# Performance work log

Hardware: AMD Instinct MI355X
Metric: run time of the kernel (lower is better)

## Reference

```python
import jax, jax.numpy as jnp
import numpy as np

B, NB, K, C, CM, POS = 8, 1024, 9, 32, 128, 2
SIGMA = 0.5
NEG_SLOPE = 0.01  # nn.LeakyReLU default
BN_EPS = 1e-5


def _leaky(x):
    return jnp.where(x >= 0, x, NEG_SLOPE * x)


def _batchnorm(x, gamma, beta):
    # BatchNorm1d, training-mode batch statistics over the point dimension
    mu = jnp.mean(x, axis=0)
    var = jnp.mean((x - mu) ** 2, axis=0)
    return gamma * (x - mu) * jax.lax.rsqrt(var + BN_EPS) + beta


def setup_inputs() -> dict:
    key = jax.random.key(0)
    ks = jax.random.split(key, 8)
    N = B * NB
    positions = jax.random.normal(ks[0], (N, POS), jnp.float32)
    weights = jax.random.normal(ks[1], (N, C), jnp.float32)
    batch = jnp.full((B,), NB, dtype=jnp.int32)  # uniform point counts per graph
    # KernelConv params: kernel_init='grid' -> 3x3 grid of offsets spanning +-sigma
    g = jnp.linspace(-SIGMA, SIGMA, 3, dtype=jnp.float32)
    kernel_positions = jnp.stack(jnp.meshgrid(g, g, indexing='ij'), axis=-1).reshape(K, POS)
    kernel_weights = (jax.random.normal(ks[2], (K, C, C), jnp.float32) / np.float32(np.sqrt(C * K)))
    conv_norm_gamma = jnp.ones((C,), jnp.float32)
    conv_norm_beta = jnp.zeros((C,), jnp.float32)
    # PyG MLP([C, CM, C+POS], act_first=True, plain_last=True)
    W1 = jax.random.normal(ks[3], (C, CM), jnp.float32) / np.float32(np.sqrt(C))
    b1 = jnp.zeros((CM,), jnp.float32)
    bn_gamma = jnp.ones((CM,), jnp.float32)
    bn_beta = jnp.zeros((CM,), jnp.float32)
    W2 = jax.random.normal(ks[4], (CM, C + POS), jnp.float32) / np.float32(np.sqrt(CM))
    b2 = jnp.zeros((C + POS,), jnp.float32)
    return dict(positions=positions, weights=weights, batch=batch,
                kernel_positions=kernel_positions, kernel_weights=kernel_weights,
                conv_norm_gamma=conv_norm_gamma, conv_norm_beta=conv_norm_beta,
                W1=W1, b1=b1, bn_gamma=bn_gamma, bn_beta=bn_beta, W2=W2, b2=b2)


def reference(positions, weights, batch, kernel_positions, kernel_weights,
              conv_norm_gamma, conv_norm_beta, W1, b1, bn_gamma, bn_beta, W2, b2):
    N = positions.shape[0]
    # --- KernelConv: each point spawns K components at pos + kernel offset ---
    conv_pos = (positions[:, None, :] + kernel_positions[None, :, :])  # [N,K,2]
    conv_w = jnp.einsum('nc,kcd->nkd', weights, kernel_weights)        # [N,K,C]
    conv_pos = conv_pos.reshape(B, NB * K, POS)
    conv_w = conv_w.reshape(B, NB * K, C)
    # --- KernelSample: evaluate Gaussian mixture at original positions ---
    p = positions.reshape(B, NB, POS)
    d2 = (jnp.sum(p * p, -1)[:, :, None]
          + jnp.sum(conv_pos * conv_pos, -1)[:, None, :]
          - 2.0 * jnp.einsum('bnd,bmd->bnm', p, conv_pos))             # [B,NB,NB*K]
    Kmat = jnp.exp(-d2 / (2.0 * SIGMA * SIGMA))
    sampled = jnp.einsum('bnm,bmc->bnc', Kmat, conv_w).reshape(N, C)
    x = _leaky(sampled)                                                 # KernelSample nonlinearity
    # conv_norm + residual add of input weights
    x = _batchnorm(x, conv_norm_gamma, conv_norm_beta) + weights
    # MLP: lin -> act -> batchnorm (act_first) -> plain last lin
    h = _batchnorm(_leaky(x @ W1 + b1), bn_gamma, bn_beta)
    mlp_out = h @ W2 + b2                                               # [N, POS + C]
    delta_pos, delta_w = mlp_out[:, :POS], mlp_out[:, POS:]
    return positions + delta_pos, x + delta_w
```

## Files before the change

kernel.cpp:

```cpp
#include <hip/hip_runtime.h>
#include <hip/hip_bf16.h>

#define BB    8
#define NBB   1024
#define KK    9
#define CC    32
#define CMM   128
#define NTOT  (BB*NBB)
#define MM    (NBB*KK)
#define MS    16
#define MR    (MM/MS)
#define NEG   0.01f
#define EPS   1e-5f
#define L2C   (-2.8853900817779268f)

#define OFF_CWT   0
#define SZ_CWT    (BB*CC*MM/2)
#define OFF_CFX   (OFF_CWT + SZ_CWT)
#define OFF_CFY   (OFF_CFX + BB*MM)
#define OFF_CF0   (OFF_CFY + BB*MM)
#define OFF_PART  (OFF_CF0 + BB*MM)
#define SZ_ONE    (NTOT*CC)
#define SZ_PART   (MS*SZ_ONE)
#define OFF_X0    (OFF_PART)
#define OFF_X     (OFF_PART + SZ_ONE)
#define OFF_H0    (OFF_PART + 2*SZ_ONE)
#define OFF_ST    (OFF_PART + SZ_PART)

typedef __attribute__((ext_vector_type(8))) short short8;
typedef __attribute__((ext_vector_type(4))) float f32x4;
typedef __attribute__((ext_vector_type(2))) float f32x2;

static __device__ __forceinline__ unsigned short f2bf_rne(float f) {
    __hip_bfloat16 h = __float2bfloat16(f);
    return *reinterpret_cast<unsigned short*>(&h);
}

__global__ __launch_bounds__(256) void k_convw(const float* __restrict__ pos,
                                               const float* __restrict__ kpos,
                                               const float* __restrict__ w,
                                               const float* __restrict__ kw,
                                               float* __restrict__ cfx,
                                               float* __restrict__ cfy,
                                               float* __restrict__ cf0,
                                               float* __restrict__ stats,
                                               short* __restrict__ cwT) {
    __shared__ unsigned short tile[4*32*144];
    __shared__ unsigned short kwl[KK*CC*CC];
    int t = threadIdx.x;
    int l = t & 63, wv = t >> 6;
    int lane15 = l & 15, quad = l >> 4;
    int blk = blockIdx.x;
    int b = blk >> 4, nbl = blk & 15;
    int n = b*NBB + nbl*64 + wv*16 + lane15;

    if (blk == 0 && t < 320) stats[t] = 0.f;
    #pragma unroll
    for (int rep = 0; rep < 3; ++rep) {
        int gid = blk*256 + t + rep*32768;
        if (gid < BB*MM) {
            int bb = gid / MM;
            int m = gid - bb*MM;
            int np = m / 9, k9 = m - np*9;
            float qx = pos[((size_t)(bb*NBB + np))*2 + 0] + kpos[k9*2 + 0];
            float qy = pos[((size_t)(bb*NBB + np))*2 + 1] + kpos[k9*2 + 1];
            cfx[gid] = -2.f*L2C*qx;
            cfy[gid] = -2.f*L2C*qy;
            cf0[gid] = L2C*(qx*qx + qy*qy);
        }
    }

    for (int u = t; u < KK*CC*CC/4; u += 256) {
        int flat = u*4;
        int row  = flat >> 5;
        int c0   = flat & 31;
        int kk = row >> 5, cp = row & 31;
        f32x4 v = *(const f32x4*)&kw[flat];
        kwl[(kk*CC + c0+0)*CC + cp] = f2bf_rne(v.x);
        kwl[(kk*CC + c0+1)*CC + cp] = f2bf_rne(v.y);
        kwl[(kk*CC + c0+2)*CC + cp] = f2bf_rne(v.z);
        kwl[(kk*CC + c0+3)*CC + cp] = f2bf_rne(v.w);
    }

    f32x4 w0 = *(const f32x4*)&w[(size_t)n*CC + quad*8];
    f32x4 w1 = *(const f32x4*)&w[(size_t)n*CC + quad*8 + 4];
    union { unsigned short us[8]; short8 s; } bfr;
    bfr.us[0] = f2bf_rne(w0.x); bfr.us[1] = f2bf_rne(w0.y);
    bfr.us[2] = f2bf_rne(w0.z); bfr.us[3] = f2bf_rne(w0.w);
    bfr.us[4] = f2bf_rne(w1.x); bfr.us[5] = f2bf_rne(w1.y);
    bfr.us[6] = f2bf_rne(w1.z); bfr.us[7] = f2bf_rne(w1.w);

    __syncthreads();

    f32x4 acc[KK][2];
    #pragma unroll
    for (int kk = 0; kk < KK; ++kk) {
        #pragma unroll
        for (int ct = 0; ct < 2; ++ct) {
            int c = ct*16 + lane15;
            short8 afr = *(const short8*)&kwl[(kk*CC + c)*CC + quad*8];
            acc[kk][ct] = __builtin_amdgcn_mfma_f32_16x16x32_bf16(
                afr, bfr.s, (f32x4)0.f, 0, 0, 0);
        }
    }
    unsigned short* tw = tile + wv*4608;
    #pragma unroll
    for (int kk = 0; kk < KK; ++kk)
        #pragma unroll
        for (int ct = 0; ct < 2; ++ct)
            #pragma unroll
            for (int reg = 0; reg < 4; ++reg) {
                int c = ct*16 + quad*4 + reg;
                tw[c*144 + lane15*9 + kk] = f2bf_rne(acc[kk][ct][reg]);
            }
    __syncthreads();
    short* dst = cwT + (size_t)b*CC*MM + (size_t)(nbl*64 + wv*16)*9;
    #pragma unroll
    for (int it = 0; it < 9; ++it) {
        int u = it*64 + l;
        int c = u / 18, seg = u - c*18;
        short8 v = *(const short8*)&tw[c*144 + seg*8];
        *(short8*)&dst[(size_t)c*MM + seg*8] = v;
    }
}

__global__ __launch_bounds__(256) void k_sample(const float* __restrict__ pos,
                                                const float* __restrict__ cfx,
                                                const float* __restrict__ cfy,
                                                const float* __restrict__ cf0,
                                                const short* __restrict__ cwT,
                                                float* __restrict__ part) {
    int t = threadIdx.x;
    int l = t & 63, w = t >> 6;
    int blk = blockIdx.x;
    int ks = blk & 15, nb = (blk >> 4) & 7, b = blk >> 7;
    int lane15 = l & 15, quad = l >> 4;
    int nbase = b*NBB + nb*128 + w*32;

    float px[2], py[2], cn[2];
    #pragma unroll
    for (int nt = 0; nt < 2; ++nt) {
        int n = nbase + nt*16 + lane15;
        float x = pos[(size_t)n*2], y = pos[(size_t)n*2 + 1];
        px[nt] = x; py[nt] = y; cn[nt] = L2C*(x*x + y*y);
    }
    f32x4 acc[2][2];
    #pragma unroll
    for (int nt = 0; nt < 2; ++nt) { acc[nt][0] = (f32x4)0.f; acc[nt][1] = (f32x4)0.f; }

    const float* bx = cfx + (size_t)b*MM;
    const float* by = cfy + (size_t)b*MM;
    const float* b0 = cf0 + (size_t)b*MM;
    const short* ca0 = cwT + (size_t)b*CC*MM + (size_t)lane15*MM;
    const short* ca1 = ca0 + (size_t)16*MM;

    int m0 = ks*MR + quad*8;
    #pragma unroll 2
    for (int kk = 0; kk < MR/32; ++kk, m0 += 32) {
        short8 a0 = *(const short8*)&ca0[m0];
        short8 a1 = *(const short8*)&ca1[m0];
        f32x4 vx0 = *(const f32x4*)&bx[m0];
        f32x4 vx1 = *(const f32x4*)&bx[m0 + 4];
        f32x4 vy0 = *(const f32x4*)&by[m0];
        f32x4 vy1 = *(const f32x4*)&by[m0 + 4];
        f32x4 v00 = *(const f32x4*)&b0[m0];
        f32x4 v01 = *(const f32x4*)&b0[m0 + 4];
        #pragma unroll
        for (int nt = 0; nt < 2; ++nt) {
            f32x2 Xv = {px[nt], px[nt]};
            f32x2 Yv = {py[nt], py[nt]};
            f32x2 Cv = {cn[nt], cn[nt]};
            f32x2 t0 = (f32x2){v00.x, v00.y} + Cv;
            t0 = (f32x2){vy0.x, vy0.y}*Yv + t0;
            t0 = (f32x2){vx0.x, vx0.y}*Xv + t0;
            f32x2 t1 = (f32x2){v00.z, v00.w} + Cv;
            t1 = (f32x2){vy0.z, vy0.w}*Yv + t1;
            t1 = (f32x2){vx0.z, vx0.w}*Xv + t1;
            f32x2 t2 = (f32x2){v01.x, v01.y} + Cv;
            t2 = (f32x2){vy1.x, vy1.y}*Yv + t2;
            t2 = (f32x2){vx1.x, vx1.y}*Xv + t2;
            f32x2 t3 = (f32x2){v01.z, v01.w} + Cv;
            t3 = (f32x2){vy1.z, vy1.w}*Yv + t3;
            t3 = (f32x2){vx1.z, vx1.w}*Xv + t3;
            float e0 = __builtin_amdgcn_exp2f(t0.x);
            float e1 = __builtin_amdgcn_exp2f(t0.y);
            float e2 = __builtin_amdgcn_exp2f(t1.x);
            float e3 = __builtin_amdgcn_exp2f(t1.y);
            float e4 = __builtin_amdgcn_exp2f(t2.x);
            float e5 = __builtin_amdgcn_exp2f(t2.y);
            float e6 = __builtin_amdgcn_exp2f(t3.x);
            float e7 = __builtin_amdgcn_exp2f(t3.y);
            union { unsigned int u[4]; short8 s; } bf;
            bf.u[0] = (__float_as_uint(e0) >> 16) | (__float_as_uint(e1) & 0xffff0000u);
            bf.u[1] = (__float_as_uint(e2) >> 16) | (__float_as_uint(e3) & 0xffff0000u);
            bf.u[2] = (__float_as_uint(e4) >> 16) | (__float_as_uint(e5) & 0xffff0000u);
            bf.u[3] = (__float_as_uint(e6) >> 16) | (__float_as_uint(e7) & 0xffff0000u);
            acc[nt][0] = __builtin_amdgcn_mfma_f32_16x16x32_bf16(a0, bf.s, acc[nt][0], 0, 0, 0);
            acc[nt][1] = __builtin_amdgcn_mfma_f32_16x16x32_bf16(a1, bf.s, acc[nt][1], 0, 0, 0);
        }
    }
    #pragma unroll
    for (int nt = 0; nt < 2; ++nt) {
        int n = nbase + nt*16 + lane15;
        #pragma unroll
        for (int ct = 0; ct < 2; ++ct) {
            int c = ct*16 + quad*4;
            *(f32x4*)&part[((size_t)ks*NTOT + n)*CC + c] = acc[nt][ct];
        }
    }
}

__global__ __launch_bounds__(256) void k_leaky_stats(const float* __restrict__ part,
                                                     float* __restrict__ x0,
                                                     float* __restrict__ s1) {
    __shared__ float ss[32], sq[32];
    int t = threadIdx.x;
    if (t < 32) { ss[t] = 0.f; sq[t] = 0.f; }
    __syncthreads();
    float lsum = 0.f, lsq = 0.f;
    int base = blockIdx.x * 1024;
    for (int j = 0; j < 4; ++j) {
        int idx = base + j*256 + t;
        float v = 0.f;
        #pragma unroll
        for (int s = 0; s < MS; ++s) v += part[(size_t)s*SZ_ONE + idx];
        v = v >= 0.f ? v : NEG*v;
        x0[idx] = v;
        lsum += v; lsq = fmaf(v, v, lsq);
    }
    atomicAdd(&ss[t & 31], lsum);
    atomicAdd(&sq[t & 31], lsq);
    __syncthreads();
    if (t < 32) { atomicAdd(&s1[t], ss[t]); atomicAdd(&s1[32+t], sq[t]); }
}

__global__ __launch_bounds__(256) void k_mlp1(const float* __restrict__ x0,
                                              const float* __restrict__ wts,
                                              const float* __restrict__ gma,
                                              const float* __restrict__ bta,
                                              const float* __restrict__ W1,
                                              const float* __restrict__ b1,
                                              const float* __restrict__ s1,
                                              float* __restrict__ x,
                                              float* __restrict__ h0,
                                              float* __restrict__ s2) {
    __shared__ float tile[64*68];
    int t = threadIdx.x;
    int l = t & 63, w = t >> 6;
    int blk = blockIdx.x;
    int nb = blk >> 1, jh = blk & 1;
    int n = nb*64 + l;
    int j0 = jh*64 + w*16;

    float xv[32];
    #pragma unroll
    for (int c = 0; c < 32; ++c) {
        float mu  = s1[c] * (1.f/NTOT);
        float var = s1[32+c]*(1.f/NTOT) - mu*mu;
        float a   = gma[c] * rsqrtf(var + EPS);
        float v   = x0[(size_t)n*CC + c];
        xv[c] = a*(v - mu) + bta[c] + wts[(size_t)n*CC + c];
    }
    if (jh == 0 && w == 0) {
        #pragma unroll
        for (int c = 0; c < 32; c += 4)
            *(float4*)&x[(size_t)n*CC + c] = make_float4(xv[c], xv[c+1], xv[c+2], xv[c+3]);
    }
    float acc[16];
    #pragma unroll
    for (int jj = 0; jj < 16; ++jj) acc[jj] = b1[j0 + jj];
    #pragma unroll 4
    for (int c = 0; c < 32; ++c) {
        float xc = xv[c];
        const float* w1r = W1 + c*CMM + j0;
        #pragma unroll
        for (int jj = 0; jj < 16; ++jj)
            acc[jj] = fmaf(xc, w1r[jj], acc[jj]);
    }
    float* hd = h0 + (size_t)n*CMM + j0;
    #pragma unroll
    for (int jj = 0; jj < 16; ++jj) {
        acc[jj] = acc[jj] >= 0.f ? acc[jj] : NEG*acc[jj];
        tile[(w*16 + jj)*68 + l] = acc[jj];
    }
    #pragma unroll
    for (int jj = 0; jj < 16; jj += 4)
        *(float4*)&hd[jj] = make_float4(acc[jj], acc[jj+1], acc[jj+2], acc[jj+3]);
    __syncthreads();
    int jl = t >> 2, grp = t & 3;
    float lsum = 0.f, lsq = 0.f;
    #pragma unroll
    for (int q = 0; q < 4; ++q) {
        f32x4 v = *(const f32x4*)&tile[jl*68 + grp*16 + q*4];
        lsum += v.x + v.y + v.z + v.w;
        lsq = fmaf(v.x, v.x, fmaf(v.y, v.y, fmaf(v.z, v.z, fmaf(v.w, v.w, lsq))));
    }
    lsum += __shfl_xor(lsum, 1); lsq += __shfl_xor(lsq, 1);
    lsum += __shfl_xor(lsum, 2); lsq += __shfl_xor(lsq, 2);
    if (grp == 0) {
        int jg = jh*64 + jl;
        atomicAdd(&s2[jg], lsum);
        atomicAdd(&s2[CMM + jg], lsq);
    }
}

__global__ __launch_bounds__(256) void k_mlp2(const float* __restrict__ h0,
                                              const float* __restrict__ x,
                                              const float* __restrict__ pos,
                                              const float* __restrict__ g2,
                                              const float* __restrict__ bt2,
                                              const float* __restrict__ W2,
                                              const float* __restrict__ b2,
                                              const float* __restrict__ s2,
                                              float* __restrict__ out) {
    __shared__ float red[8][32][35];
    int t = threadIdx.x;
    int lane = t & 63, w = t >> 6;
    int half = lane >> 5;
    int nl = lane & 31;
    int n = blockIdx.x*32 + nl;
    int j0 = w*32 + half*16;
    float hv[16];
    #pragma unroll
    for (int q = 0; q < 4; ++q)
        *(float4*)&hv[q*4] = *(const float4*)&h0[(size_t)n*CMM + j0 + q*4];
    #pragma unroll
    for (int jj = 0; jj < 16; ++jj) {
        int j = j0 + jj;
        float mu  = s2[j] * (1.f/NTOT);
        float var = s2[CMM+j]*(1.f/NTOT) - mu*mu;
        float a   = g2[j] * rsqrtf(var + EPS);
        hv[jj] = a*(hv[jj] - mu) + bt2[j];
    }
    float acc[34];
    #pragma unroll
    for (int c = 0; c < 34; ++c) acc[c] = 0.f;
    for (int jj = 0; jj < 16; ++jj) {
        float h = hv[jj];
        const float* w2r = W2 + (size_t)(j0 + jj)*34;
        #pragma unroll
        for (int c = 0; c < 34; ++c)
            acc[c] = fmaf(h, w2r[c], acc[c]);
    }
    int rid = w*2 + half;
    #pragma unroll
    for (int c = 0; c < 34; ++c) red[rid][nl][c] = acc[c];
    __syncthreads();
    for (int u = t; u < 32*34; u += 256) {
        int r = u / 34, c = u - r*34;
        float v = red[0][r][c] + red[1][r][c] + red[2][r][c] + red[3][r][c]
                + red[4][r][c] + red[5][r][c] + red[6][r][c] + red[7][r][c] + b2[c];
        int nn = blockIdx.x*32 + r;
        if (c < 2)
            out[(size_t)nn*2 + c] = pos[(size_t)nn*2 + c] + v;
        else
            out[16384 + (size_t)nn*32 + (c-2)] = x[(size_t)nn*32 + (c-2)] + v;
    }
}

extern "C" void kernel_launch(void* const* d_in, const int* in_sizes, int n_in,
                              void* d_out, int out_size, void* d_ws, size_t ws_size,
                              hipStream_t stream) {
    const float* positions = (const float*)d_in[0];
    const float* weights   = (const float*)d_in[1];
    const float* kpos = (const float*)d_in[3];
    const float* kw   = (const float*)d_in[4];
    const float* cg   = (const float*)d_in[5];
    const float* cb   = (const float*)d_in[6];
    const float* W1   = (const float*)d_in[7];
    const float* b1   = (const float*)d_in[8];
    const float* bg   = (const float*)d_in[9];
    const float* bb   = (const float*)d_in[10];
    const float* W2   = (const float*)d_in[11];
    const float* b2   = (const float*)d_in[12];
    float* ws  = (float*)d_ws;
    float* out = (float*)d_out;

    float* s1 = ws + OFF_ST;
    float* s2 = ws + OFF_ST + 64;

    k_convw<<<128, 256, 0, stream>>>(positions, kpos, weights, kw,
                                     ws + OFF_CFX, ws + OFF_CFY, ws + OFF_CF0,
                                     s1, (short*)(ws + OFF_CWT));
    k_sample<<<1024, 256, 0, stream>>>(positions, ws + OFF_CFX, ws + OFF_CFY,
                                       ws + OFF_CF0, (const short*)(ws + OFF_CWT),
                                       ws + OFF_PART);
    k_leaky_stats<<<256, 256, 0, stream>>>(ws + OFF_PART, ws + OFF_X0, s1);
    k_mlp1<<<256, 256, 0, stream>>>(ws + OFF_X0, weights, cg, cb, W1, b1,
                                    s1, ws + OFF_X, ws + OFF_H0, s2);
    k_mlp2<<<256, 256, 0, stream>>>(ws + OFF_H0, ws + OFF_X, positions,
                                    bg, bb, W2, b2, s2, out);
}
```

Measured before the change: 159.2 us.

## Fuse split-K reduction and leaky/stats into sample kernel; rebalance grids

The sampling kernel now uses 1024-thread blocks in which 16 waves split the M dimension for 32 points. The partial results are reduced in shared memory, then leaky-ReLU, the x0 write and the BN statistics are applied in the same kernel. This removes the separate leaky_stats kernel and its 16x partial-sum round trip through global memory. The convw, mlp1 and mlp2 kernels are regridded to smaller tiles with more blocks to improve parallelism. The cost is fewer sample blocks (256), which may lower occupancy and latency hiding.

```diff
diff --git a/kernel.cpp b/kernel.cpp
--- a/kernel.cpp
+++ b/kernel.cpp
@@ -8,8 +8,6 @@
 #define CMM   128
 #define NTOT  (BB*NBB)
 #define MM    (NBB*KK)
-#define MS    16
-#define MR    (MM/MS)
 #define NEG   0.01f
 #define EPS   1e-5f
 #define L2C   (-2.8853900817779268f)
@@ -19,13 +17,10 @@
 #define OFF_CFX   (OFF_CWT + SZ_CWT)
 #define OFF_CFY   (OFF_CFX + BB*MM)
 #define OFF_CF0   (OFF_CFY + BB*MM)
-#define OFF_PART  (OFF_CF0 + BB*MM)
-#define SZ_ONE    (NTOT*CC)
-#define SZ_PART   (MS*SZ_ONE)
-#define OFF_X0    (OFF_PART)
-#define OFF_X     (OFF_PART + SZ_ONE)
-#define OFF_H0    (OFF_PART + 2*SZ_ONE)
-#define OFF_ST    (OFF_PART + SZ_PART)
+#define OFF_X0    (OFF_CF0 + BB*MM)
+#define OFF_X     (OFF_X0 + NTOT*CC)
+#define OFF_H0    (OFF_X + NTOT*CC)
+#define OFF_ST    (OFF_H0 + NTOT*CMM)
 
 typedef __attribute__((ext_vector_type(8))) short short8;
 typedef __attribute__((ext_vector_type(4))) float f32x4;
@@ -45,19 +40,18 @@
                                                float* __restrict__ cf0,
                                                float* __restrict__ stats,
                                                short* __restrict__ cwT) {
-    __shared__ unsigned short tile[4*32*144];
     __shared__ unsigned short kwl[KK*CC*CC];
+    __shared__ unsigned short tile[2*32*144];
     int t = threadIdx.x;
     int l = t & 63, wv = t >> 6;
     int lane15 = l & 15, quad = l >> 4;
     int blk = blockIdx.x;
-    int b = blk >> 4, nbl = blk & 15;
-    int n = b*NBB + nbl*64 + wv*16 + lane15;
+    int b = blk & 7, nbl = blk >> 3;
 
     if (blk == 0 && t < 320) stats[t] = 0.f;
     #pragma unroll
-    for (int rep = 0; rep < 3; ++rep) {
-        int gid = blk*256 + t + rep*32768;
+    for (int rep = 0; rep < 2; ++rep) {
+        int gid = rep*65536 + blk*256 + t;
         if (gid < BB*MM) {
             int bb = gid / MM;
             int m = gid - bb*MM;
@@ -69,11 +63,10 @@
             cf0[gid] = L2C*(qx*qx + qy*qy);
         }
     }
-
     for (int u = t; u < KK*CC*CC/4; u += 256) {
         int flat = u*4;
-        int row  = flat >> 5;
-        int c0   = flat & 31;
+        int row = flat >> 5;
+        int c0 = flat & 31;
         int kk = row >> 5, cp = row & 31;
         f32x4 v = *(const f32x4*)&kw[flat];
         kwl[(kk*CC + c0+0)*CC + cp] = f2bf_rne(v.x);
@@ -81,7 +74,7 @@
         kwl[(kk*CC + c0+2)*CC + cp] = f2bf_rne(v.z);
         kwl[(kk*CC + c0+3)*CC + cp] = f2bf_rne(v.w);
     }
-
+    int n = b*NBB + nbl*32 + (wv & 1)*16 + lane15;
     f32x4 w0 = *(const f32x4*)&w[(size_t)n*CC + quad*8];
     f32x4 w1 = *(const f32x4*)&w[(size_t)n*CC + quad*8 + 4];
     union { unsigned short us[8]; short8 s; } bfr;
@@ -89,53 +82,60 @@
     bfr.us[2] = f2bf_rne(w0.z); bfr.us[3] = f2bf_rne(w0.w);
     bfr.us[4] = f2bf_rne(w1.x); bfr.us[5] = f2bf_rne(w1.y);
     bfr.us[6] = f2bf_rne(w1.z); bfr.us[7] = f2bf_rne(w1.w);
-
-    __syncthreads();
-
-    f32x4 acc[KK][2];
-    #pragma unroll
-    for (int kk = 0; kk < KK; ++kk) {
-        #pragma unroll
-        for (int ct = 0; ct < 2; ++ct) {
-            int c = ct*16 + lane15;
-            short8 afr = *(const short8*)&kwl[(kk*CC + c)*CC + quad*8];
-            acc[kk][ct] = __builtin_amdgcn_mfma_f32_16x16x32_bf16(
-                afr, bfr.s, (f32x4)0.f, 0, 0, 0);
-        }
-    }
-    unsigned short* tw = tile + wv*4608;
-    #pragma unroll
-    for (int kk = 0; kk < KK; ++kk)
-        #pragma unroll
-        for (int ct = 0; ct < 2; ++ct)
+    __syncthreads();
+    if (wv < 2) {
+        f32x4 acc[KK][2];
+        #pragma unroll
+        for (int kk = 0; kk < KK; ++kk)
             #pragma unroll
-            for (int reg = 0; reg < 4; ++reg) {
-                int c = ct*16 + quad*4 + reg;
-                tw[c*144 + lane15*9 + kk] = f2bf_rne(acc[kk][ct][reg]);
+            for (int ct = 0; ct < 2; ++ct) {
+                int c = ct*16 + lane15;
+                short8 afr = *(const short8*)&kwl[(kk*CC + c)*CC + quad*8];
+                acc[kk][ct] = __builtin_amdgcn_mfma_f32_16x16x32_bf16(
+                    afr, bfr.s, (f32x4)0.f, 0, 0, 0);
             }
-    __syncthreads();
-    short* dst = cwT + (size_t)b*CC*MM + (size_t)(nbl*64 + wv*16)*9;
-    #pragma unroll
-    for (int it = 0; it < 9; ++it) {
-        int u = it*64 + l;
-        int c = u / 18, seg = u - c*18;
-        short8 v = *(const short8*)&tw[c*144 + seg*8];
-        *(short8*)&dst[(size_t)c*MM + seg*8] = v;
-    }
-}
-
-__global__ __launch_bounds__(256) void k_sample(const float* __restrict__ pos,
-                                                const float* __restrict__ cfx,
-                                                const float* __restrict__ cfy,
-                                                const float* __restrict__ cf0,
-                                                const short* __restrict__ cwT,
-                                                float* __restrict__ part) {
+        unsigned short* tw = tile + wv*4608;
+        #pragma unroll
+        for (int kk = 0; kk < KK; ++kk)
+            #pragma unroll
+            for (int ct = 0; ct < 2; ++ct)
+                #pragma unroll
+                for (int reg = 0; reg < 4; ++reg) {
+                    int c = ct*16 + quad*4 + reg;
+                    tw[c*144 + lane15*9 + kk] = f2bf_rne(acc[kk][ct][reg]);
+                }
+    }
+    __syncthreads();
+    short* dst = cwT + (size_t)b*CC*MM + (size_t)(nbl*32)*9;
+    #pragma unroll
+    for (int it = 0; it < 5; ++it) {
+        int u = it*256 + t;
+        if (u < 1152) {
+            int c = u / 36, seg = u - c*36;
+            const unsigned short* src = tile + (seg < 18 ? 0 : 4608)
+                                      + c*144 + (seg < 18 ? seg : seg - 18)*8;
+            short8 v = *(const short8*)src;
+            *(short8*)&dst[(size_t)c*MM + seg*8] = v;
+        }
+    }
+}
+
+__global__ __launch_bounds__(1024) void k_sample(const float* __restrict__ pos,
+                                                 const float* __restrict__ cfx,
+                                                 const float* __restrict__ cfy,
+                                                 const float* __restrict__ cf0,
+                                                 const short* __restrict__ cwT,
+                                                 float* __restrict__ x0,
+                                                 float* __restrict__ s1) {
+    __shared__ float red[16*32*36];
+    __shared__ float sstat[64];
     int t = threadIdx.x;
-    int l = t & 63, w = t >> 6;
+    int l = t & 63, wv = t >> 6;
     int blk = blockIdx.x;
-    int ks = blk & 15, nb = (blk >> 4) & 7, b = blk >> 7;
+    int b = blk & 7, nblk = blk >> 3;
     int lane15 = l & 15, quad = l >> 4;
-    int nbase = b*NBB + nb*128 + w*32;
+    int nbase = b*NBB + nblk*32;
+    if (t < 64) sstat[t] = 0.f;
 
     float px[2], py[2], cn[2];
     #pragma unroll
@@ -145,8 +145,8 @@
         px[nt] = x; py[nt] = y; cn[nt] = L2C*(x*x + y*y);
     }
     f32x4 acc[2][2];
-    #pragma unroll
-    for (int nt = 0; nt < 2; ++nt) { acc[nt][0] = (f32x4)0.f; acc[nt][1] = (f32x4)0.f; }
+    acc[0][0] = (f32x4)0.f; acc[0][1] = (f32x4)0.f;
+    acc[1][0] = (f32x4)0.f; acc[1][1] = (f32x4)0.f;
 
     const float* bx = cfx + (size_t)b*MM;
     const float* by = cfy + (size_t)b*MM;
@@ -154,9 +154,9 @@
     const short* ca0 = cwT + (size_t)b*CC*MM + (size_t)lane15*MM;
     const short* ca1 = ca0 + (size_t)16*MM;
 
-    int m0 = ks*MR + quad*8;
+    int m0 = wv*576 + quad*8;
     #pragma unroll 2
-    for (int kk = 0; kk < MR/32; ++kk, m0 += 32) {
+    for (int kk = 0; kk < 18; ++kk, m0 += 32) {
         short8 a0 = *(const short8*)&ca0[m0];
         short8 a1 = *(const short8*)&ca1[m0];
         f32x4 vx0 = *(const f32x4*)&bx[m0];
@@ -200,38 +200,42 @@
         }
     }
     #pragma unroll
-    for (int nt = 0; nt < 2; ++nt) {
-        int n = nbase + nt*16 + lane15;
+    for (int nt = 0; nt < 2; ++nt)
         #pragma unroll
         for (int ct = 0; ct < 2; ++ct) {
-            int c = ct*16 + quad*4;
-            *(f32x4*)&part[((size_t)ks*NTOT + n)*CC + c] = acc[nt][ct];
-        }
-    }
-}
-
-__global__ __launch_bounds__(256) void k_leaky_stats(const float* __restrict__ part,
-                                                     float* __restrict__ x0,
-                                                     float* __restrict__ s1) {
-    __shared__ float ss[32], sq[32];
-    int t = threadIdx.x;
-    if (t < 32) { ss[t] = 0.f; sq[t] = 0.f; }
-    __syncthreads();
-    float lsum = 0.f, lsq = 0.f;
-    int base = blockIdx.x * 1024;
-    for (int j = 0; j < 4; ++j) {
-        int idx = base + j*256 + t;
-        float v = 0.f;
-        #pragma unroll
-        for (int s = 0; s < MS; ++s) v += part[(size_t)s*SZ_ONE + idx];
-        v = v >= 0.f ? v : NEG*v;
-        x0[idx] = v;
-        lsum += v; lsq = fmaf(v, v, lsq);
-    }
-    atomicAdd(&ss[t & 31], lsum);
-    atomicAdd(&sq[t & 31], lsq);
-    __syncthreads();
-    if (t < 32) { atomicAdd(&s1[t], ss[t]); atomicAdd(&s1[32+t], sq[t]); }
+            int n = nt*16 + lane15, c = ct*16 + quad*4;
+            *(f32x4*)&red[(wv*32 + n)*36 + c] = acc[nt][ct];
+        }
+    __syncthreads();
+    if (t < 256) {
+        int nr = t >> 3, c0 = (t & 7)*4;
+        f32x4 v = (f32x4)0.f;
+        #pragma unroll
+        for (int wp = 0; wp < 16; ++wp)
+            v = v + *(const f32x4*)&red[(wp*32 + nr)*36 + c0];
+        v.x = v.x >= 0.f ? v.x : NEG*v.x;
+        v.y = v.y >= 0.f ? v.y : NEG*v.y;
+        v.z = v.z >= 0.f ? v.z : NEG*v.z;
+        v.w = v.w >= 0.f ? v.w : NEG*v.w;
+        *(f32x4*)&x0[((size_t)(nbase + nr))*CC + c0] = v;
+        float s0 = v.x, s1v = v.y, s2v = v.z, s3v = v.w;
+        float q0 = v.x*v.x, q1 = v.y*v.y, q2 = v.z*v.z, q3 = v.w*v.w;
+        #pragma unroll
+        for (int mk = 8; mk <= 32; mk <<= 1) {
+            s0 += __shfl_xor(s0, mk); s1v += __shfl_xor(s1v, mk);
+            s2v += __shfl_xor(s2v, mk); s3v += __shfl_xor(s3v, mk);
+            q0 += __shfl_xor(q0, mk); q1 += __shfl_xor(q1, mk);
+            q2 += __shfl_xor(q2, mk); q3 += __shfl_xor(q3, mk);
+        }
+        if (l < 8) {
+            atomicAdd(&sstat[c0 + 0], s0);  atomicAdd(&sstat[c0 + 1], s1v);
+            atomicAdd(&sstat[c0 + 2], s2v); atomicAdd(&sstat[c0 + 3], s3v);
+            atomicAdd(&sstat[32 + c0 + 0], q0); atomicAdd(&sstat[32 + c0 + 1], q1);
+            atomicAdd(&sstat[32 + c0 + 2], q2); atomicAdd(&sstat[32 + c0 + 3], q3);
+        }
+    }
+    __syncthreads();
+    if (t < 64) atomicAdd(&s1[t], sstat[t]);
 }
 
 __global__ __launch_bounds__(256) void k_mlp1(const float* __restrict__ x0,
@@ -244,13 +248,13 @@
                                               float* __restrict__ x,
                                               float* __restrict__ h0,
                                               float* __restrict__ s2) {
-    __shared__ float tile[64*68];
+    __shared__ float tile[32*68];
     int t = threadIdx.x;
-    int l = t & 63, w = t >> 6;
+    int l = t & 63, wv = t >> 6;
     int blk = blockIdx.x;
-    int nb = blk >> 1, jh = blk & 1;
+    int nb = blk >> 2, jq = blk & 3;
     int n = nb*64 + l;
-    int j0 = jh*64 + w*16;
+    int j0 = jq*32 + wv*8;
 
     float xv[32];
     #pragma unroll
@@ -261,46 +265,51 @@
         float v   = x0[(size_t)n*CC + c];
         xv[c] = a*(v - mu) + bta[c] + wts[(size_t)n*CC + c];
     }
-    if (jh == 0 && w == 0) {
+    if (jq == 0 && wv == 0) {
         #pragma unroll
         for (int c = 0; c < 32; c += 4)
             *(float4*)&x[(size_t)n*CC + c] = make_float4(xv[c], xv[c+1], xv[c+2], xv[c+3]);
     }
-    float acc[16];
-    #pragma unroll
-    for (int jj = 0; jj < 16; ++jj) acc[jj] = b1[j0 + jj];
-    #pragma unroll 4
+    float acc[8];
+    *(f32x4*)&acc[0] = *(const f32x4*)&b1[j0];
+    *(f32x4*)&acc[4] = *(const f32x4*)&b1[j0 + 4];
+    #pragma unroll 8
     for (int c = 0; c < 32; ++c) {
         float xc = xv[c];
         const float* w1r = W1 + c*CMM + j0;
-        #pragma unroll
-        for (int jj = 0; jj < 16; ++jj)
-            acc[jj] = fmaf(xc, w1r[jj], acc[jj]);
+        f32x4 wa = *(const f32x4*)&w1r[0];
+        f32x4 wb = *(const f32x4*)&w1r[4];
+        acc[0] = fmaf(xc, wa.x, acc[0]); acc[1] = fmaf(xc, wa.y, acc[1]);
+        acc[2] = fmaf(xc, wa.z, acc[2]); acc[3] = fmaf(xc, wa.w, acc[3]);
+        acc[4] = fmaf(xc, wb.x, acc[4]); acc[5] = fmaf(xc, wb.y, acc[5]);
+        acc[6] = fmaf(xc, wb.z, acc[6]); acc[7] = fmaf(xc, wb.w, acc[7]);
+    }
+    #pragma unroll
+    for (int jj = 0; jj < 8; ++jj) {
+        acc[jj] = acc[jj] >= 0.f ? acc[jj] : NEG*acc[jj];
+        tile[(wv*8 + jj)*68 + l] = acc[jj];
     }
     float* hd = h0 + (size_t)n*CMM + j0;
-    #pragma unroll
-    for (int jj = 0; jj < 16; ++jj) {
-        acc[jj] = acc[jj] >= 0.f ? acc[jj] : NEG*acc[jj];
-        tile[(w*16 + jj)*68 + l] = acc[jj];
-    }
-    #pragma unroll
-    for (int jj = 0; jj < 16; jj += 4)
-        *(float4*)&hd[jj] = make_float4(acc[jj], acc[jj+1], acc[jj+2], acc[jj+3]);
-    __syncthreads();
-    int jl = t >> 2, grp = t & 3;
-    float lsum = 0.f, lsq = 0.f;
-    #pragma unroll
-    for (int q = 0; q < 4; ++q) {
-        f32x4 v = *(const f32x4*)&tile[jl*68 + grp*16 + q*4];
-        lsum += v.x + v.y + v.z + v.w;
-        lsq = fmaf(v.x, v.x, fmaf(v.y, v.y, fmaf(v.z, v.z, fmaf(v.w, v.w, lsq))));
-    }
-    lsum += __shfl_xor(lsum, 1); lsq += __shfl_xor(lsq, 1);
-    lsum += __shfl_xor(lsum, 2); lsq += __shfl_xor(lsq, 2);
-    if (grp == 0) {
-        int jg = jh*64 + jl;
-        atomicAdd(&s2[jg], lsum);
-        atomicAdd(&s2[CMM + jg], lsq);
+    *(float4*)&hd[0] = make_float4(acc[0], acc[1], acc[2], acc[3]);
+    *(float4*)&hd[4] = make_float4(acc[4], acc[5], acc[6], acc[7]);
+    __syncthreads();
+    if (t < 256) {
+        int jl = t >> 3, grp = t & 7;
+        float lsum = 0.f, lsq = 0.f;
+        #pragma unroll
+        for (int q = 0; q < 2; ++q) {
+            f32x4 v = *(const f32x4*)&tile[jl*68 + grp*8 + q*4];
+            lsum += v.x + v.y + v.z + v.w;
+            lsq = fmaf(v.x, v.x, fmaf(v.y, v.y, fmaf(v.z, v.z, fmaf(v.w, v.w, lsq))));
+        }
+        lsum += __shfl_xor(lsum, 1); lsq += __shfl_xor(lsq, 1);
+        lsum += __shfl_xor(lsum, 2); lsq += __shfl_xor(lsq, 2);
+        lsum += __shfl_xor(lsum, 4); lsq += __shfl_xor(lsq, 4);
+        if (grp == 0) {
+            int jg = jq*32 + jl;
+            atomicAdd(&s2[jg], lsum);
+            atomicAdd(&s2[CMM + jg], lsq);
+        }
     }
 }
 
@@ -313,19 +322,16 @@
                                               const float* __restrict__ b2,
                                               const float* __restrict__ s2,
                                               float* __restrict__ out) {
-    __shared__ float red[8][32][35];
+    __shared__ float red[16*16*35];
     int t = threadIdx.x;
-    int lane = t & 63, w = t >> 6;
-    int half = lane >> 5;
-    int nl = lane & 31;
-    int n = blockIdx.x*32 + nl;
-    int j0 = w*32 + half*16;
-    float hv[16];
-    #pragma unroll
-    for (int q = 0; q < 4; ++q)
-        *(float4*)&hv[q*4] = *(const float4*)&h0[(size_t)n*CMM + j0 + q*4];
-    #pragma unroll
-    for (int jj = 0; jj < 16; ++jj) {
+    int nl = t & 15, rid = t >> 4;
+    int n = blockIdx.x*16 + nl;
+    int j0 = rid*8;
+    float hv[8];
+    *(f32x4*)&hv[0] = *(const f32x4*)&h0[(size_t)n*CMM + j0];
+    *(f32x4*)&hv[4] = *(const f32x4*)&h0[(size_t)n*CMM + j0 + 4];
+    #pragma unroll
+    for (int jj = 0; jj < 8; ++jj) {
         int j = j0 + jj;
         float mu  = s2[j] * (1.f/NTOT);
         float var = s2[CMM+j]*(1.f/NTOT) - mu*mu;
@@ -335,26 +341,30 @@
     float acc[34];
     #pragma unroll
     for (int c = 0; c < 34; ++c) acc[c] = 0.f;
-    for (int jj = 0; jj < 16; ++jj) {
+    for (int jj = 0; jj < 8; ++jj) {
         float h = hv[jj];
         const float* w2r = W2 + (size_t)(j0 + jj)*34;
         #pragma unroll
         for (int c = 0; c < 34; ++c)
             acc[c] = fmaf(h, w2r[c], acc[c]);
     }
-    int rid = w*2 + half;
-    #pragma unroll
-    for (int c = 0; c < 34; ++c) red[rid][nl][c] = acc[c];
-    __syncthreads();
-    for (int u = t; u < 32*34; u += 256) {
-        int r = u / 34, c = u - r*34;
-        float v = red[0][r][c] + red[1][r][c] + red[2][r][c] + red[3][r][c]
-                + red[4][r][c] + red[5][r][c] + red[6][r][c] + red[7][r][c] + b2[c];
-        int nn = blockIdx.x*32 + r;
-        if (c < 2)
-            out[(size_t)nn*2 + c] = pos[(size_t)nn*2 + c] + v;
-        else
-            out[16384 + (size_t)nn*32 + (c-2)] = x[(size_t)nn*32 + (c-2)] + v;
+    #pragma unroll
+    for (int c = 0; c < 34; ++c) red[(rid*16 + nl)*35 + c] = acc[c];
+    __syncthreads();
+    #pragma unroll
+    for (int it = 0; it < 3; ++it) {
+        int u = it*256 + t;
+        if (u < 544) {
+            int r = u / 34, c = u - r*34;
+            float v = b2[c];
+            #pragma unroll
+            for (int rr = 0; rr < 16; ++rr) v += red[(rr*16 + r)*35 + c];
+            int nn = blockIdx.x*16 + r;
+            if (c < 2)
+                out[(size_t)nn*2 + c] = pos[(size_t)nn*2 + c] + v;
+            else
+                out[16384 + (size_t)nn*32 + (c-2)] = x[(size_t)nn*32 + (c-2)] + v;
+        }
     }
 }
 
@@ -379,15 +389,14 @@
     float* s1 = ws + OFF_ST;
     float* s2 = ws + OFF_ST + 64;
 
-    k_convw<<<128, 256, 0, stream>>>(positions, kpos, weights, kw,
+    k_convw<<<256, 256, 0, stream>>>(positions, kpos, weights, kw,
                                      ws + OFF_CFX, ws + OFF_CFY, ws + OFF_CF0,
                                      s1, (short*)(ws + OFF_CWT));
-    k_sample<<<1024, 256, 0, stream>>>(positions, ws + OFF_CFX, ws + OFF_CFY,
+    k_sample<<<256, 1024, 0, stream>>>(positions, ws + OFF_CFX, ws + OFF_CFY,
                                        ws + OFF_CF0, (const short*)(ws + OFF_CWT),
-                                       ws + OFF_PART);
-    k_leaky_stats<<<256, 256, 0, stream>>>(ws + OFF_PART, ws + OFF_X0, s1);
-    k_mlp1<<<256, 256, 0, stream>>>(ws + OFF_X0, weights, cg, cb, W1, b1,
+                                       ws + OFF_X0, s1);
+    k_mlp1<<<512, 256, 0, stream>>>(ws + OFF_X0, weights, cg, cb, W1, b1,
                                     s1, ws + OFF_X, ws + OFF_H0, s2);
-    k_mlp2<<<256, 256, 0, stream>>>(ws + OFF_H0, ws + OFF_X, positions,
+    k_mlp2<<<512, 256, 0, stream>>>(ws + OFF_H0, ws + OFF_X, positions,
                                     bg, bb, W2, b2, s2, out);
 }
```

Result: faster. 154.1 us (-3.2%).
